# Kernel optimization log

Measured on AMD Instinct MI355X. Metric: run time of the kernel, lower is better.

The kernel has to match this reference:

```python
import jax, jax.numpy as jnp
import numpy as np

B, H, S, D = 4, 16, 2048, 128
D_MODEL = 128  # scale factor per module init


def setup_inputs() -> dict:
    key = jax.random.key(0)
    kq, kk, kv = jax.random.split(key, 3)
    Q = jax.random.normal(kq, (B, H, S, D), dtype=jnp.float32)
    K = jax.random.normal(kk, (B, H, S, D), dtype=jnp.float32)
    V = jax.random.normal(kv, (B, H, S, D), dtype=jnp.float32)
    return {"Q": Q, "K": K, "V": V}


def reference(Q, K, V):
    # scores: [B, H, S, S]
    scores = jnp.einsum("bhqd,bhkd->bhqk", Q, K) / np.sqrt(D_MODEL).astype(np.float32)
    # causal mask: lower-triangular keeps, upper becomes -inf
    q_idx = jnp.arange(S)[:, None]
    k_idx = jnp.arange(S)[None, :]
    causal = q_idx >= k_idx  # [S, S]
    scores = jnp.where(causal, scores, -jnp.inf)
    attn = jax.nn.softmax(scores, axis=-1)
    return jnp.einsum("bhqk,bhkd->bhqd", attn, V)
```

## Files before the change

### kernel.cpp

```cpp
#include <hip/hip_runtime.h>

typedef _Float16 f16;
typedef _Float16 f16x4 __attribute__((ext_vector_type(4)));
typedef _Float16 f16x8 __attribute__((ext_vector_type(8)));
typedef float    f32x16 __attribute__((ext_vector_type(16)));
typedef int      i32x4 __attribute__((ext_vector_type(4)));

#define B_ 4
#define H_ 16
#define S_ 2048
#define D_ 128
#define KVB 32
#define KSTR 136
#define VTSTR 40

union U4 { i32x4 i; f16x8 h; };

__device__ __forceinline__ unsigned pk2(float a, float b) {
    auto v = __builtin_amdgcn_cvt_pkrtz(a, b);
    return __builtin_bit_cast(unsigned, v);
}

__device__ __forceinline__ f16x8 cvt8(const float4 a, const float4 b) {
    f16x8 h;
    h[0] = (f16)a.x; h[1] = (f16)a.y; h[2] = (f16)a.z; h[3] = (f16)a.w;
    h[4] = (f16)b.x; h[5] = (f16)b.y; h[6] = (f16)b.z; h[7] = (f16)b.w;
    return h;
}

__global__ __launch_bounds__(256)
void prep(const float* __restrict__ K, const float* __restrict__ V,
          f16* __restrict__ Kh, f16* __restrict__ Vtt)
{
    const int bid = blockIdx.x;
    const int bh  = bid >> 5;
    const int kb  = bid & 31;
    const int k0  = kb * 64;
    const int tid = threadIdx.x;

    const float* Kb = K + ((size_t)bh * S_ + k0) * D_;
    const float* Vb = V + ((size_t)bh * S_ + k0) * D_;
    f16* Khb = Kh + ((size_t)bh * S_ + k0) * D_;
    f16* Vtb = Vtt + (size_t)bh * S_ * D_ + (size_t)kb * 2 * (D_ * 32);

    #pragma unroll
    for (int it = 0; it < 4; ++it) {
        const int idx = tid + it * 256;
        const int row = idx >> 4, c8 = idx & 15;
        const float4 a = *(const float4*)(Kb + row * D_ + c8 * 8);
        const float4 b = *(const float4*)(Kb + row * D_ + c8 * 8 + 4);
        *(f16x8*)(Khb + row * D_ + c8 * 8) = cvt8(a, b);
    }
    #pragma unroll
    for (int it = 0; it < 4; ++it) {
        const int idx = tid + it * 256;
        const int d  = idx & 127;
        const int k8 = idx >> 7;
        const float* vp = Vb + (size_t)(k8 * 8) * D_ + d;
        f16x4 lo, hi;
        #pragma unroll
        for (int e = 0; e < 4; ++e) lo[e] = (f16)vp[(size_t)e * D_];
        #pragma unroll
        for (int e = 0; e < 4; ++e) hi[e] = (f16)vp[(size_t)(e + 4) * D_];
        f16* dst = Vtb + (size_t)(k8 >> 2) * (D_ * 32) + d * 32
                 + ((k8 >> 1) & 1) * 16 + (k8 & 1) * 4;
        *(f16x4*)(dst)     = lo;
        *(f16x4*)(dst + 8) = hi;
    }
}

__global__ __launch_bounds__(256, 2)
void fattn13(const float* __restrict__ Qg, const f16* __restrict__ Khg,
             const f16* __restrict__ Vttg, float* __restrict__ Og)
{
    __shared__ __align__(16) f16 Klds[3][KVB * KSTR];
    __shared__ __align__(16) f16 Vt[3][128 * VTSTR];

    const int id  = blockIdx.x;
    const int xcd = id & 7;
    const int r   = id >> 3;
    const int bh  = xcd + 8 * (r & 7);
    const int p   = r >> 3;

    const int tid  = threadIdx.x;
    const int lane = tid & 63;
    const int l31  = lane & 31;
    const int h    = lane >> 5;
    const int wv   = tid >> 6;

    const float* Qb  = Qg   + (size_t)bh * S_ * D_;
    const f16*   Khb = Khg  + (size_t)bh * S_ * D_;
    const f16*   Vtb = Vttg + (size_t)bh * S_ * D_;
    float*       Ob  = Og   + (size_t)bh * S_ * D_;

    const f16* kS = Khb + (tid >> 4) * D_ + (tid & 15) * 8;
    const f16* vS = Vtb + (size_t)tid * 8;
    const int  kDo = (tid >> 4) * KSTR + (tid & 15) * 8;
    const int  vDo = (tid >> 2) * VTSTR + (tid & 3) * 8;

    i32x4 kr[2], vr[2];
    auto issue = [&](int kt) {
        const f16* kp = kS + ((size_t)kt << 12);
        const f16* vp = vS + ((size_t)kt << 12);
        kr[0] = *(const i32x4*)kp;
        kr[1] = *(const i32x4*)(kp + 2048);
        vr[0] = *(const i32x4*)vp;
        vr[1] = *(const i32x4*)(vp + 2048);
    };
    auto writeLds = [&](int buf) {
        f16* kb = &Klds[buf][0];
        f16* vb = &Vt[buf][0];
        *(i32x4*)(kb + kDo)              = kr[0];
        *(i32x4*)(kb + kDo + 16 * KSTR)  = kr[1];
        *(i32x4*)(vb + vDo)              = vr[0];
        *(i32x4*)(vb + vDo + 64 * VTSTR) = vr[1];
    };
    f16x8 qf[8];
    auto qkt = [&](int buf) {
        f32x16 a;
        #pragma unroll
        for (int rr = 0; rr < 16; ++rr) a[rr] = 0.f;
        #pragma unroll
        for (int dc = 0; dc < 8; ++dc) {
            const f16x8 kf = *(const f16x8*)&Klds[buf][l31 * KSTR + dc * 16 + h * 8];
            a = __builtin_amdgcn_mfma_f32_32x32x16_f16(kf, qf[dc], a, 0, 0, 0);
        }
        return a;
    };

    const float qmul = 0.08838834764831845f * 1.4426950408889634f;

    #pragma unroll 1
    for (int ph = 0; ph < 2; ++ph) {
        const int qt  = ph ? 15 - p : p;
        const int qw0 = qt * 128 + wv * 32;
        const int qg  = qw0 + l31;
        const int nkt = 4 * qt + 4;
        const int lastt = 4 * qt + wv;

        {
            const float* Qrow = Qb + (size_t)(qw0 + l31) * D_;
            #pragma unroll
            for (int dc = 0; dc < 8; ++dc) {
                const float4 a = *(const float4*)(Qrow + dc * 16 + h * 8);
                const float4 b = *(const float4*)(Qrow + dc * 16 + h * 8 + 4);
                f16x8 q;
                q[0] = (f16)(a.x * qmul); q[1] = (f16)(a.y * qmul);
                q[2] = (f16)(a.z * qmul); q[3] = (f16)(a.w * qmul);
                q[4] = (f16)(b.x * qmul); q[5] = (f16)(b.y * qmul);
                q[6] = (f16)(b.z * qmul); q[7] = (f16)(b.w * qmul);
                qf[dc] = q;
            }
        }

        f32x16 acc[4];
        #pragma unroll
        for (int dt = 0; dt < 4; ++dt)
            #pragma unroll
            for (int rr = 0; rr < 16; ++rr) acc[dt][rr] = 0.f;
        float m_i = -1e30f, l_i = 0.f;

        __syncthreads();
        issue(0);  writeLds(0);
        issue(1);  writeLds(1);
        if (nkt > 2) issue(2);
        __syncthreads();
        f32x16 sv = qkt(0);

        int bB = 0, bA = 1, bW = 2;
        for (int kt = 0; kt < nkt; ++kt) {
            __syncthreads();
            if (kt + 2 < nkt) {
                writeLds(bW);
                if (kt + 3 < nkt) issue(kt + 3);
            }

            __builtin_amdgcn_s_setprio(1);
            f32x16 svn;
            if (kt + 1 < nkt && kt + 1 <= lastt) svn = qkt(bA);

            if (kt <= lastt) {
                const int k0 = kt * KVB;
                if (k0 + 31 > qw0) {
                    #pragma unroll
                    for (int rr = 0; rr < 16; ++rr) {
                        const int kg = k0 + (rr & 3) + 8 * (rr >> 2) + 4 * h;
                        if (kg > qg) sv[rr] = -1e30f;
                    }
                }
                const float m1 = fmaxf(fmaxf(sv[0], sv[1]), sv[2]);
                const float m2 = fmaxf(fmaxf(sv[3], sv[4]), sv[5]);
                const float m3 = fmaxf(fmaxf(sv[6], sv[7]), sv[8]);
                const float m4 = fmaxf(fmaxf(sv[9], sv[10]), sv[11]);
                const float m5 = fmaxf(fmaxf(sv[12], sv[13]), sv[14]);
                float mx = fmaxf(fmaxf(m1, m2), m3);
                mx = fmaxf(fmaxf(mx, m4), m5);
                mx = fmaxf(mx, sv[15]);
                mx = fmaxf(mx, __shfl_xor(mx, 32));
                if (!__all(mx - m_i <= 8.0f)) {
                    const float mn = fmaxf(m_i, mx);
                    const float al = exp2f(m_i - mn);
                    m_i = mn;
                    l_i *= al;
                    float arow[16];
                    #pragma unroll
                    for (int rr = 0; rr < 16; ++rr)
                        arow[rr] = __shfl(al, (rr & 3) + 8 * (rr >> 2) + 4 * h);
                    #pragma unroll
                    for (int dt = 0; dt < 4; ++dt)
                        #pragma unroll
                        for (int rr = 0; rr < 16; ++rr) acc[dt][rr] *= arow[rr];
                }
                #pragma unroll
                for (int rr = 0; rr < 16; ++rr) sv[rr] = exp2f(sv[rr] - m_i);
                float s8[8];
                #pragma unroll
                for (int rr = 0; rr < 8; ++rr) s8[rr] = sv[2 * rr] + sv[2 * rr + 1];
                #pragma unroll
                for (int rr = 0; rr < 4; ++rr) s8[rr] += s8[rr + 4];
                s8[0] += s8[2]; s8[1] += s8[3];
                float rs = s8[0] + s8[1];
                rs += __shfl_xor(rs, 32);
                l_i += rs;
                U4 pa[2];
                #pragma unroll
                for (int m = 0; m < 4; ++m) pa[0].i[m] = (int)pk2(sv[2 * m],     sv[2 * m + 1]);
                #pragma unroll
                for (int m = 0; m < 4; ++m) pa[1].i[m] = (int)pk2(sv[8 + 2 * m], sv[9 + 2 * m]);
                #pragma unroll
                for (int dt = 0; dt < 4; ++dt) {
                    const f16* vrow = &Vt[bB][(dt * 32 + l31) * VTSTR + h * 8];
                    const f16x8 vb0 = *(const f16x8*)(vrow + 0);
                    const f16x8 vb1 = *(const f16x8*)(vrow + 16);
                    acc[dt] = __builtin_amdgcn_mfma_f32_32x32x16_f16(pa[0].h, vb0, acc[dt], 0, 0, 0);
                    acc[dt] = __builtin_amdgcn_mfma_f32_32x32x16_f16(pa[1].h, vb1, acc[dt], 0, 0, 0);
                }
            }
            __builtin_amdgcn_s_setprio(0);

            if (kt + 1 < nkt) sv = svn;
            const int t = bB; bB = bA; bA = bW; bW = t;
        }

        float li[16];
        #pragma unroll
        for (int rr = 0; rr < 16; ++rr) {
            const float lv = __shfl(l_i, (rr & 3) + 8 * (rr >> 2) + 4 * h);
            li[rr] = 1.0f / lv;
        }
        #pragma unroll
        for (int dt = 0; dt < 4; ++dt)
            #pragma unroll
            for (int rr = 0; rr < 16; ++rr) {
                const int row = qw0 + (rr & 3) + 8 * (rr >> 2) + 4 * h;
                Ob[(size_t)row * D_ + dt * 32 + l31] = acc[dt][rr] * li[rr];
            }
    }
}

__global__ __launch_bounds__(256, 3)
void fattn5(const float* __restrict__ Qg, const float* __restrict__ Kg,
            const float* __restrict__ Vg, float* __restrict__ Og)
{
    __shared__ __align__(16) f16 Klds[2][KVB * KSTR];
    __shared__ __align__(16) f16 Vt[2][128 * VTSTR];
    const int id  = blockIdx.x;
    const int xcd = id & 7;
    const int w   = id >> 3;
    const int qt  = 15 - (w & 15);
    const int bh  = xcd + 8 * (w >> 4);
    const int tid  = threadIdx.x;
    const int lane = tid & 63;
    const int wv   = tid >> 6;
    const int l31  = lane & 31;
    const int h    = lane >> 5;
    const int qw0 = qt * 128 + wv * 32;
    const int qg  = qw0 + l31;
    const size_t base = (size_t)bh * S_ * D_;
    const float* Qb = Qg + base;
    const float* Kb = Kg + base;
    const float* Vb = Vg + base;
    float*       Ob = Og + base;
    const int nkt = 4 * qt + 4;
    float4 kr[4];
    float  vr[16];
    auto issue = [&](int kt) {
        const int k0n = kt * KVB;
        #pragma unroll
        for (int it = 0; it < 2; ++it) {
            const int idx  = tid + it * 256;
            const int krow = idx >> 4;
            const int c8   = idx & 15;
            const float* kp = Kb + (size_t)(k0n + krow) * D_ + c8 * 8;
            kr[it * 2]     = *(const float4*)kp;
            kr[it * 2 + 1] = *(const float4*)(kp + 4);
            const int d  = idx & 127;
            const int k8 = idx >> 7;
            const float* vp = Vb + (size_t)(k0n + k8 * 8) * D_ + d;
            #pragma unroll
            for (int e = 0; e < 8; ++e) vr[it * 8 + e] = vp[(size_t)e * D_];
        }
    };
    auto writeLds = [&](int buf) {
        #pragma unroll
        for (int it = 0; it < 2; ++it) {
            const int idx  = tid + it * 256;
            const int krow = idx >> 4;
            const int c8   = idx & 15;
            *(f16x8*)&Klds[buf][krow * KSTR + c8 * 8] = cvt8(kr[it * 2], kr[it * 2 + 1]);
            const int d  = idx & 127;
            const int k8 = idx >> 7;
            f16x8 vh;
            #pragma unroll
            for (int e = 0; e < 8; ++e) vh[e] = (f16)vr[it * 8 + e];
            *(f16x8*)&Vt[buf][d * VTSTR + k8 * 8] = vh;
        }
    };
    const float qmul = 0.08838834764831845f * 1.4426950408889634f;
    f16x8 qf[8];
    {
        const float* Qrow = Qb + (size_t)(qw0 + l31) * D_;
        #pragma unroll
        for (int dc = 0; dc < 8; ++dc) {
            const float4 a = *(const float4*)(Qrow + dc * 16 + h * 8);
            const float4 b = *(const float4*)(Qrow + dc * 16 + h * 8 + 4);
            f16x8 q;
            q[0] = (f16)(a.x * qmul); q[1] = (f16)(a.y * qmul);
            q[2] = (f16)(a.z * qmul); q[3] = (f16)(a.w * qmul);
            q[4] = (f16)(b.x * qmul); q[5] = (f16)(b.y * qmul);
            q[6] = (f16)(b.z * qmul); q[7] = (f16)(b.w * qmul);
            qf[dc] = q;
        }
    }
    f32x16 acc[4];
    #pragma unroll
    for (int dt = 0; dt < 4; ++dt)
        #pragma unroll
        for (int rr = 0; rr < 16; ++rr) acc[dt][rr] = 0.f;
    float m_i = -1e30f, l_i = 0.f;
    issue(0);
    writeLds(0);
    if (nkt > 1) issue(1);
    __syncthreads();
    for (int kt = 0; kt < nkt; ++kt) {
        const int k0  = kt * KVB;
        const int cur = kt & 1;
        if (k0 <= qw0 + 31) {
            f32x16 sv;
            #pragma unroll
            for (int rr = 0; rr < 16; ++rr) sv[rr] = 0.f;
            #pragma unroll
            for (int dc = 0; dc < 8; ++dc) {
                const f16x8 kf = *(const f16x8*)&Klds[cur][l31 * KSTR + dc * 16 + h * 8];
                sv = __builtin_amdgcn_mfma_f32_32x32x16_f16(kf, qf[dc], sv, 0, 0, 0);
            }
            if (k0 + 31 > qw0) {
                #pragma unroll
                for (int rr = 0; rr < 16; ++rr) {
                    const int kg = k0 + (rr & 3) + 8 * (rr >> 2) + 4 * h;
                    if (kg > qg) sv[rr] = -1e30f;
                }
            }
            float mx = sv[0];
            #pragma unroll
            for (int rr = 1; rr < 16; ++rr) mx = fmaxf(mx, sv[rr]);
            mx = fmaxf(mx, __shfl_xor(mx, 32));
            if (!__all(mx - m_i <= 8.0f)) {
                const float mn = fmaxf(m_i, mx);
                const float al = exp2f(m_i - mn);
                m_i = mn;
                l_i *= al;
                float arow[16];
                #pragma unroll
                for (int rr = 0; rr < 16; ++rr)
                    arow[rr] = __shfl(al, (rr & 3) + 8 * (rr >> 2) + 4 * h);
                #pragma unroll
                for (int dt = 0; dt < 4; ++dt)
                    #pragma unroll
                    for (int rr = 0; rr < 16; ++rr) acc[dt][rr] *= arow[rr];
            }
            float rs = 0.f;
            #pragma unroll
            for (int rr = 0; rr < 16; ++rr) {
                sv[rr] = exp2f(sv[rr] - m_i);
                rs += sv[rr];
            }
            rs += __shfl_xor(rs, 32);
            l_i += rs;
            U4 pa[2];
            {
                unsigned dwp[8];
                #pragma unroll
                for (int m = 0; m < 8; ++m) dwp[m] = pk2(sv[2 * m], sv[2 * m + 1]);
                #pragma unroll
                for (int hf = 0; hf < 2; ++hf) {
                    const unsigned a0 = dwp[hf * 4 + 0], a1 = dwp[hf * 4 + 1];
                    const unsigned b0 = dwp[hf * 4 + 2], b1 = dwp[hf * 4 + 3];
                    const unsigned sa0 = (unsigned)__shfl_xor((int)a0, 32);
                    const unsigned sa1 = (unsigned)__shfl_xor((int)a1, 32);
                    const unsigned sb0 = (unsigned)__shfl_xor((int)b0, 32);
                    const unsigned sb1 = (unsigned)__shfl_xor((int)b1, 32);
                    i32x4 d;
                    d[0] = h ? (int)sb0 : (int)a0;
                    d[1] = h ? (int)sb1 : (int)a1;
                    d[2] = h ? (int)b0  : (int)sa0;
                    d[3] = h ? (int)b1  : (int)sa1;
                    pa[hf].i = d;
                }
            }
            #pragma unroll
            for (int dt = 0; dt < 4; ++dt) {
                const f16* vrow = &Vt[cur][(dt * 32 + l31) * VTSTR + h * 8];
                const f16x8 vb0 = *(const f16x8*)(vrow + 0);
                const f16x8 vb1 = *(const f16x8*)(vrow + 16);
                acc[dt] = __builtin_amdgcn_mfma_f32_32x32x16_f16(pa[0].h, vb0, acc[dt], 0, 0, 0);
                acc[dt] = __builtin_amdgcn_mfma_f32_32x32x16_f16(pa[1].h, vb1, acc[dt], 0, 0, 0);
            }
        }
        if (kt + 1 < nkt) {
            writeLds(cur ^ 1);
            if (kt + 2 < nkt) issue(kt + 2);
            __syncthreads();
        }
    }
    float li[16];
    #pragma unroll
    for (int rr = 0; rr < 16; ++rr) {
        const float lv = __shfl(l_i, (rr & 3) + 8 * (rr >> 2) + 4 * h);
        li[rr] = 1.0f / lv;
    }
    #pragma unroll
    for (int dt = 0; dt < 4; ++dt)
        #pragma unroll
        for (int rr = 0; rr < 16; ++rr) {
            const int row = qw0 + (rr & 3) + 8 * (rr >> 2) + 4 * h;
            Ob[(size_t)row * D_ + dt * 32 + l31] = acc[dt][rr] * li[rr];
        }
}

extern "C" void kernel_launch(void* const* d_in, const int* in_sizes, int n_in,
                              void* d_out, int out_size, void* d_ws, size_t ws_size,
                              hipStream_t stream) {
    (void)in_sizes; (void)n_in; (void)out_size;
    const float* Q = (const float*)d_in[0];
    const float* K = (const float*)d_in[1];
    const float* V = (const float*)d_in[2];
    float* O = (float*)d_out;
    const size_t elems  = (size_t)B_ * H_ * S_ * D_;
    const size_t needKV = elems * 2 * sizeof(f16);
    if (ws_size >= needKV) {
        f16* Kh  = (f16*)d_ws;
        f16* Vtt = Kh + elems;
        prep<<<dim3(B_ * H_ * (S_ / 64)), dim3(256), 0, stream>>>(K, V, Kh, Vtt);
        fattn13<<<dim3(512), dim3(256), 0, stream>>>(Q, Kh, Vtt, O);
    } else {
        fattn5<<<dim3((S_ / 128) * B_ * H_), dim3(256), 0, stream>>>(Q, K, V, O);
    }
}
```

Measured before the change: 161.7 us.

## Defer the PV MFMA by one tile and widen the V-transpose stores

The P·V matmul for tile kt-1 is now issued in iteration kt, alongside the QK^T of the next tile and the softmax of the current one. This overlaps MFMA work with the exp and reduction code. The tile is finished off in an epilogue after the loop. The packed P fragments are carried across iterations in registers. LDS buffers grow from 3 to 4, indexed by the tile number modulo 4, so the deferred tile's V stays resident. The prep kernel now writes the transposed V as a single 8-wide f16 store with a permuted key order instead of two 4-wide stores. This costs extra LDS and register pressure, which could limit occupancy at 2 blocks per CU.

```diff
diff --git a/kernel.cpp b/kernel.cpp
--- a/kernel.cpp
+++ b/kernel.cpp
@@ -1,7 +1,6 @@
 #include <hip/hip_runtime.h>
 
 typedef _Float16 f16;
-typedef _Float16 f16x4 __attribute__((ext_vector_type(4)));
 typedef _Float16 f16x8 __attribute__((ext_vector_type(8)));
 typedef float    f32x16 __attribute__((ext_vector_type(16)));
 typedef int      i32x4 __attribute__((ext_vector_type(4)));
@@ -56,25 +55,27 @@
         const int idx = tid + it * 256;
         const int d  = idx & 127;
         const int k8 = idx >> 7;
-        const float* vp = Vb + (size_t)(k8 * 8) * D_ + d;
-        f16x4 lo, hi;
-        #pragma unroll
-        for (int e = 0; e < 4; ++e) lo[e] = (f16)vp[(size_t)e * D_];
-        #pragma unroll
-        for (int e = 0; e < 4; ++e) hi[e] = (f16)vp[(size_t)(e + 4) * D_];
-        f16* dst = Vtb + (size_t)(k8 >> 2) * (D_ * 32) + d * 32
-                 + ((k8 >> 1) & 1) * 16 + (k8 & 1) * 4;
-        *(f16x4*)(dst)     = lo;
-        *(f16x4*)(dst + 8) = hi;
+        const int t  = k8 >> 2;
+        const int o  = k8 & 3;
+        const int c  = o >> 1, odd = o & 1;
+        const int kbase = t * 32 + c * 16 + odd * 4;
+        const float* vp0 = Vb + (size_t)kbase * D_ + d;
+        const float* vp1 = vp0 + (size_t)8 * D_;
+        f16x8 vh;
+        #pragma unroll
+        for (int e = 0; e < 4; ++e) vh[e] = (f16)vp0[(size_t)e * D_];
+        #pragma unroll
+        for (int e = 0; e < 4; ++e) vh[4 + e] = (f16)vp1[(size_t)e * D_];
+        *(f16x8*)(Vtb + (size_t)t * (D_ * 32) + d * 32 + o * 8) = vh;
     }
 }
 
 __global__ __launch_bounds__(256, 2)
-void fattn13(const float* __restrict__ Qg, const f16* __restrict__ Khg,
+void fattn15(const float* __restrict__ Qg, const f16* __restrict__ Khg,
              const f16* __restrict__ Vttg, float* __restrict__ Og)
 {
-    __shared__ __align__(16) f16 Klds[3][KVB * KSTR];
-    __shared__ __align__(16) f16 Vt[3][128 * VTSTR];
+    __shared__ __align__(16) f16 Klds[4][KVB * KSTR];
+    __shared__ __align__(16) f16 Vt[4][128 * VTSTR];
 
     const int id  = blockIdx.x;
     const int xcd = id & 7;
@@ -167,17 +168,30 @@
         __syncthreads();
         f32x16 sv = qkt(0);
 
-        int bB = 0, bA = 1, bW = 2;
+        U4 pa0c, pa1c, pa0p, pa1p;
+
         for (int kt = 0; kt < nkt; ++kt) {
             __syncthreads();
             if (kt + 2 < nkt) {
-                writeLds(bW);
+                writeLds((kt + 2) & 3);
                 if (kt + 3 < nkt) issue(kt + 3);
             }
 
             __builtin_amdgcn_s_setprio(1);
             f32x16 svn;
-            if (kt + 1 < nkt && kt + 1 <= lastt) svn = qkt(bA);
+            const bool doA = (kt + 1 < nkt) && (kt + 1 <= lastt);
+            if (doA) svn = qkt((kt + 1) & 3);
+
+            if (kt >= 1 && kt - 1 <= lastt) {
+                const f16* vbase = &Vt[(kt - 1) & 3][l31 * VTSTR + h * 8];
+                #pragma unroll
+                for (int dt = 0; dt < 4; ++dt) {
+                    const f16x8 vb0 = *(const f16x8*)(vbase + dt * 32 * VTSTR);
+                    const f16x8 vb1 = *(const f16x8*)(vbase + dt * 32 * VTSTR + 16);
+                    acc[dt] = __builtin_amdgcn_mfma_f32_32x32x16_f16(pa0p.h, vb0, acc[dt], 0, 0, 0);
+                    acc[dt] = __builtin_amdgcn_mfma_f32_32x32x16_f16(pa1p.h, vb1, acc[dt], 0, 0, 0);
+                }
+            }
 
             if (kt <= lastt) {
                 const int k0 = kt * KVB;
@@ -222,24 +236,26 @@
                 float rs = s8[0] + s8[1];
                 rs += __shfl_xor(rs, 32);
                 l_i += rs;
-                U4 pa[2];
-                #pragma unroll
-                for (int m = 0; m < 4; ++m) pa[0].i[m] = (int)pk2(sv[2 * m],     sv[2 * m + 1]);
-                #pragma unroll
-                for (int m = 0; m < 4; ++m) pa[1].i[m] = (int)pk2(sv[8 + 2 * m], sv[9 + 2 * m]);
-                #pragma unroll
-                for (int dt = 0; dt < 4; ++dt) {
-                    const f16* vrow = &Vt[bB][(dt * 32 + l31) * VTSTR + h * 8];
-                    const f16x8 vb0 = *(const f16x8*)(vrow + 0);
-                    const f16x8 vb1 = *(const f16x8*)(vrow + 16);
-                    acc[dt] = __builtin_amdgcn_mfma_f32_32x32x16_f16(pa[0].h, vb0, acc[dt], 0, 0, 0);
-                    acc[dt] = __builtin_amdgcn_mfma_f32_32x32x16_f16(pa[1].h, vb1, acc[dt], 0, 0, 0);
-                }
+                #pragma unroll
+                for (int m = 0; m < 4; ++m) pa0c.i[m] = (int)pk2(sv[2 * m],     sv[2 * m + 1]);
+                #pragma unroll
+                for (int m = 0; m < 4; ++m) pa1c.i[m] = (int)pk2(sv[8 + 2 * m], sv[9 + 2 * m]);
             }
             __builtin_amdgcn_s_setprio(0);
 
-            if (kt + 1 < nkt) sv = svn;
-            const int t = bB; bB = bA; bA = bW; bW = t;
+            pa0p = pa0c; pa1p = pa1c;
+            if (doA) sv = svn;
+        }
+
+        if (lastt == nkt - 1) {
+            const f16* vbase = &Vt[lastt & 3][l31 * VTSTR + h * 8];
+            #pragma unroll
+            for (int dt = 0; dt < 4; ++dt) {
+                const f16x8 vb0 = *(const f16x8*)(vbase + dt * 32 * VTSTR);
+                const f16x8 vb1 = *(const f16x8*)(vbase + dt * 32 * VTSTR + 16);
+                acc[dt] = __builtin_amdgcn_mfma_f32_32x32x16_f16(pa0p.h, vb0, acc[dt], 0, 0, 0);
+                acc[dt] = __builtin_amdgcn_mfma_f32_32x32x16_f16(pa1p.h, vb1, acc[dt], 0, 0, 0);
+            }
         }
 
         float li[16];
@@ -452,7 +468,7 @@
         f16* Kh  = (f16*)d_ws;
         f16* Vtt = Kh + elems;
         prep<<<dim3(B_ * H_ * (S_ / 64)), dim3(256), 0, stream>>>(K, V, Kh, Vtt);
-        fattn13<<<dim3(512), dim3(256), 0, stream>>>(Q, Kh, Vtt, O);
+        fattn15<<<dim3(512), dim3(256), 0, stream>>>(Q, Kh, Vtt, O);
     } else {
         fattn5<<<dim3((S_ / 128) * B_ * H_), dim3(256), 0, stream>>>(Q, K, V, O);
     }
```

Result: faster. 156.0 us (-3.5%).
